# Kernel optimization log

Hardware: AMD Instinct MI355X
Metric: run time of the kernel (lower is better)

Reference implementation:

```python
import jax, jax.numpy as jnp
import numpy as np
from jax import lax

WINDOW_SIZE = 12
POOL = 4  # AvgPool2d(4): 12x12 -> 3x3

# 4 directional 3x3 kernels, stacked as [O=4, I=1, 3, 3]
_KERNELS = np.stack([
    np.array([[0, 0, 0], [-1, 1, 0], [0, 0, 0]], np.float32),  # left
    np.array([[0, 0, 0], [0, 1, -1], [0, 0, 0]], np.float32),  # right
    np.array([[0, -1, 0], [0, 1, 0], [0, 0, 0]], np.float32),  # up
    np.array([[0, 0, 0], [0, 1, 0], [0, -1, 0]], np.float32),  # down
])[:, None, :, :]


def setup_inputs() -> dict:
    key = jax.random.key(0)
    k1, k2 = jax.random.split(key)
    windows_num = 200000
    n = WINDOW_SIZE * WINDOW_SIZE * windows_num
    samples1 = jax.random.uniform(k1, (n, 3), dtype=jnp.float32)
    samples2 = jax.random.uniform(k2, (n, 3), dtype=jnp.float32)
    return {"samples1": samples1, "samples2": samples2, "windows_num": windows_num}


def _to_pooled(samples, windows_num):
    # [W*W*N, C] -> [W, W, N, C] -> [N, C, W, W]
    x = samples.reshape(WINDOW_SIZE, WINDOW_SIZE, windows_num, -1)
    x = jnp.transpose(x, (2, 3, 0, 1))
    # channel mean, keepdim -> [N, 1, W, W]
    m = jnp.mean(x, axis=1, keepdims=True)
    # AvgPool2d(4): [N,1,12,12] -> [N,1,3,3]
    hp = WINDOW_SIZE // POOL
    p = m.reshape(windows_num, 1, hp, POOL, hp, POOL).mean(axis=(3, 5))
    return p


def _dir_grads(x):
    # x: [N,1,3,3]; 4 directional 3x3 convs, padding=1 -> [N,4,3,3]
    k = jnp.asarray(_KERNELS)
    return lax.conv_general_dilated(
        x, k, window_strides=(1, 1), padding=[(1, 1), (1, 1)],
        dimension_numbers=("NCHW", "OIHW", "NCHW"))


def reference(samples1, samples2, windows_num):
    org_pool = _to_pooled(samples1, windows_num)
    enh_pool = _to_pooled(samples2, windows_num)
    d_org = _dir_grads(org_pool)
    d_enh = _dir_grads(enh_pool)
    # squared diff per direction, summed over the 4 directions -> [N,3,3]
    E = jnp.sum((d_org - d_enh) ** 2, axis=1)
    return jnp.mean(E)
```

## Files before the change

kernel.cpp:

```cpp
#include <hip/hip_runtime.h>

__global__ __launch_bounds__(256) void spa_kernel(
    const float* __restrict__ s1, const float* __restrict__ s2,
    float* __restrict__ out, int N, float scale) {
  const int lane = threadIdx.x & 63;
  const int rg   = threadIdx.x >> 6;
  const int win  = blockIdx.x * 64 + lane;

  float rowacc[3][3];
#pragma unroll
  for (int a = 0; a < 3; ++a)
#pragma unroll
    for (int b = 0; b < 3; ++b) rowacc[a][b] = 0.f;

  if (win < N) {
    const size_t stride = (size_t)N * 3u;
    const float* p1 = s1 + (size_t)win * 3u;
    const float* p2 = s2 + (size_t)win * 3u;
#pragma unroll
    for (int ii = 0; ii < 3; ++ii) {
      const int i = rg * 3 + ii;
      const float* q1 = p1 + (size_t)(i * 12) * stride;
      const float* q2 = p2 + (size_t)(i * 12) * stride;
#pragma unroll
      for (int j = 0; j < 12; ++j) {
        const float* a = q1 + (size_t)j * stride;
        const float* b = q2 + (size_t)j * stride;
        float d = (a[0] + a[1] + a[2]) - (b[0] + b[1] + b[2]);
        rowacc[ii][j >> 2] += d;
      }
    }
  }

  __shared__ float sRow[12][64][3];
#pragma unroll
  for (int ii = 0; ii < 3; ++ii) {
    const int i = rg * 3 + ii;
#pragma unroll
    for (int c = 0; c < 3; ++c) sRow[i][lane][c] = rowacc[ii][c];
  }
  __syncthreads();

  if (rg == 0) {
    float P[9];
#pragma unroll
    for (int p = 0; p < 3; ++p)
#pragma unroll
      for (int c = 0; c < 3; ++c) {
        float v = sRow[4 * p][lane][c] + sRow[4 * p + 1][lane][c] +
                  sRow[4 * p + 2][lane][c] + sRow[4 * p + 3][lane][c];
        P[p * 3 + c] = v * (1.0f / 48.0f);
      }

    float e = 0.f;
#pragma unroll
    for (int i = 0; i < 3; ++i) {
#pragma unroll
      for (int j = 0; j < 3; ++j) {
        float c = P[i * 3 + j];
        float l = (j > 0) ? P[i * 3 + j - 1] : 0.f;
        float r = (j < 2) ? P[i * 3 + j + 1] : 0.f;
        float u = (i > 0) ? P[(i - 1) * 3 + j] : 0.f;
        float d = (i < 2) ? P[(i + 1) * 3 + j] : 0.f;
        float dl = c - l, dr = c - r, du = c - u, dd = c - d;
        e += dl * dl + dr * dr + du * du + dd * dd;
      }
    }

#pragma unroll
    for (int off = 32; off > 0; off >>= 1) e += __shfl_down(e, off, 64);
    if (lane == 0) atomicAdd(out, e * scale);
  }
}

extern "C" void kernel_launch(void* const* d_in, const int* in_sizes, int n_in,
                              void* d_out, int out_size, void* d_ws, size_t ws_size,
                              hipStream_t stream) {
  const float* s1 = (const float*)d_in[0];
  const float* s2 = (const float*)d_in[1];
  float* out = (float*)d_out;
  int N = in_sizes[0] / (12 * 12 * 3);
  float scale = 1.0f / (9.0f * (float)N);
  hipMemsetAsync(d_out, 0, sizeof(float), stream);
  int blocks = (N + 63) / 64;
  spa_kernel<<<blocks, 256, 0, stream>>>(s1, s2, out, N, scale);
}
```

Baseline: 618.2 us.

## Split reduction into vectorized partial-sum kernel and finishing kernel via workspace

Replaces the single kernel with two passes. The first launches one thread per (pooled row-slab, group of 4 windows) and uses float4 loads to sum channel differences into a workspace. The second reads the 36 partial sums per window, computes the directional gradient energy and reduces. This aims for wider, better-coalesced memory access and more parallelism, at the cost of an extra workspace write and read plus a second launch; it falls back to the old kernel if the workspace is too small.

```diff
diff --git a/kernel.cpp b/kernel.cpp
--- a/kernel.cpp
+++ b/kernel.cpp
@@ -1,18 +1,111 @@
 #include <hip/hip_runtime.h>
 
-__global__ __launch_bounds__(256) void spa_kernel(
+
+__global__ __launch_bounds__(256) void spa_partial(
+    const float* __restrict__ s1, const float* __restrict__ s2,
+    float* __restrict__ ws, int N, int Q ) {
+  const long long t = (long long)blockIdx.x * blockDim.x + threadIdx.x;
+  const int s = (int)(t / Q);
+  const int q = (int)(t % Q);
+  if (s >= 36) return;
+  const int i = s / 3;
+  const int jc = s - i * 3;
+
+  float acc0 = 0.f, acc1 = 0.f, acc2 = 0.f, acc3 = 0.f;
+  const size_t slab = (size_t)N * 3u;
+
+  if (4 * q + 3 < N) {
+    const size_t off = (size_t)q * 12u;
+#pragma unroll
+    for (int jj = 0; jj < 4; ++jj) {
+      const int p = i * 12 + jc * 4 + jj;
+      const float4* a4 = (const float4*)(s1 + (size_t)p * slab + off);
+      const float4* b4 = (const float4*)(s2 + (size_t)p * slab + off);
+      float4 a0 = a4[0], a1 = a4[1], a2 = a4[2];
+      float4 b0 = b4[0], b1 = b4[1], b2 = b4[2];
+      float4 d0 = make_float4(a0.x - b0.x, a0.y - b0.y, a0.z - b0.z, a0.w - b0.w);
+      float4 d1 = make_float4(a1.x - b1.x, a1.y - b1.y, a1.z - b1.z, a1.w - b1.w);
+      float4 d2 = make_float4(a2.x - b2.x, a2.y - b2.y, a2.z - b2.z, a2.w - b2.w);
+      acc0 += d0.x + d0.y + d0.z;
+      acc1 += d0.w + d1.x + d1.y;
+      acc2 += d1.z + d1.w + d2.x;
+      acc3 += d2.y + d2.z + d2.w;
+    }
+    float4* w4 = (float4*)(ws + (size_t)s * N + (size_t)q * 4u);
+    *w4 = make_float4(acc0, acc1, acc2, acc3);
+  } else {
+    float acc[4] = {0.f, 0.f, 0.f, 0.f};
+#pragma unroll
+    for (int jj = 0; jj < 4; ++jj) {
+      const int p = i * 12 + jc * 4 + jj;
+      const float* a = s1 + (size_t)p * slab;
+      const float* b = s2 + (size_t)p * slab;
+      for (int w = 0; w < 4; ++w) {
+        const int n = 4 * q + w;
+        if (n < N) {
+          const size_t o = (size_t)n * 3u;
+          acc[w] += (a[o] + a[o + 1] + a[o + 2]) - (b[o] + b[o + 1] + b[o + 2]);
+        }
+      }
+    }
+    for (int w = 0; w < 4; ++w) {
+      const int n = 4 * q + w;
+      if (n < N) ws[(size_t)s * N + n] = acc[w];
+    }
+  }
+}
+
+__global__ __launch_bounds__(256) void spa_finish(
+    const float* __restrict__ ws, float* __restrict__ out, int N, float scale) {
+  const int n = blockIdx.x * blockDim.x + threadIdx.x;
+  float e = 0.f;
+  if (n < N) {
+    float P[9];
+#pragma unroll
+    for (int ip = 0; ip < 3; ++ip)
+#pragma unroll
+      for (int jc = 0; jc < 3; ++jc) {
+        float v = 0.f;
+#pragma unroll
+        for (int ii = 0; ii < 4; ++ii)
+          v += ws[(size_t)((4 * ip + ii) * 3 + jc) * N + n];
+        P[ip * 3 + jc] = v * (1.0f / 48.0f);
+      }
+#pragma unroll
+    for (int i = 0; i < 3; ++i) {
+#pragma unroll
+      for (int j = 0; j < 3; ++j) {
+        float c = P[i * 3 + j];
+        float l = (j > 0) ? P[i * 3 + j - 1] : 0.f;
+        float r = (j < 2) ? P[i * 3 + j + 1] : 0.f;
+        float u = (i > 0) ? P[(i - 1) * 3 + j] : 0.f;
+        float d = (i < 2) ? P[(i + 1) * 3 + j] : 0.f;
+        float dl = c - l, dr = c - r, du = c - u, dd = c - d;
+        e += dl * dl + dr * dr + du * du + dd * dd;
+      }
+    }
+  }
+#pragma unroll
+  for (int off = 32; off > 0; off >>= 1) e += __shfl_down(e, off, 64);
+  __shared__ float sm[4];
+  const int lane = threadIdx.x & 63;
+  const int wid = threadIdx.x >> 6;
+  if (lane == 0) sm[wid] = e;
+  __syncthreads();
+  if (threadIdx.x == 0) atomicAdd(out, (sm[0] + sm[1] + sm[2] + sm[3]) * scale);
+}
+
+__global__ __launch_bounds__(256) void spa_mono(
     const float* __restrict__ s1, const float* __restrict__ s2,
     float* __restrict__ out, int N, float scale) {
   const int lane = threadIdx.x & 63;
-  const int rg   = threadIdx.x >> 6;
-  const int win  = blockIdx.x * 64 + lane;
-
+  const int rg = threadIdx.x >> 6;
+  const int win = blockIdx.x * 64 + lane;
   float rowacc[3][3];
 #pragma unroll
   for (int a = 0; a < 3; ++a)
 #pragma unroll
     for (int b = 0; b < 3; ++b) rowacc[a][b] = 0.f;
-
   if (win < N) {
     const size_t stride = (size_t)N * 3u;
     const float* p1 = s1 + (size_t)win * 3u;
@@ -31,7 +124,6 @@
       }
     }
   }
-
   __shared__ float sRow[12][64][3];
 #pragma unroll
   for (int ii = 0; ii < 3; ++ii) {
@@ -40,7 +132,6 @@
     for (int c = 0; c < 3; ++c) sRow[i][lane][c] = rowacc[ii][c];
   }
   __syncthreads();
-
   if (rg == 0) {
     float P[9];
 #pragma unroll
@@ -51,7 +142,6 @@
                   sRow[4 * p + 2][lane][c] + sRow[4 * p + 3][lane][c];
         P[p * 3 + c] = v * (1.0f / 48.0f);
       }
-
     float e = 0.f;
 #pragma unroll
     for (int i = 0; i < 3; ++i) {
@@ -66,7 +156,6 @@
         e += dl * dl + dr * dr + du * du + dd * dd;
       }
     }
-
 #pragma unroll
     for (int off = 32; off > 0; off >>= 1) e += __shfl_down(e, off, 64);
     if (lane == 0) atomicAdd(out, e * scale);
@@ -79,9 +168,20 @@
   const float* s1 = (const float*)d_in[0];
   const float* s2 = (const float*)d_in[1];
   float* out = (float*)d_out;
-  int N = in_sizes[0] / (12 * 12 * 3);
-  float scale = 1.0f / (9.0f * (float)N);
+  const int N = in_sizes[0] / (12 * 12 * 3);
+  const float scale = 1.0f / (9.0f * (float)N);
   hipMemsetAsync(d_out, 0, sizeof(float), stream);
-  int blocks = (N + 63) / 64;
-  spa_kernel<<<blocks, 256, 0, stream>>>(s1, s2, out, N, scale);
+
+  const size_t ws_needed = (size_t)36 * (size_t)N * sizeof(float);
+  if (ws_size >= ws_needed) {
+    const int Q = (N + 3) / 4;
+    const long long threads = 36LL * Q;
+    const int blocksA = (int)((threads + 255) / 256);
+    spa_partial<<<blocksA, 256, 0, stream>>>(s1, s2, (float*)d_ws, N, Q);
+    const int blocksB = (N + 255) / 256;
+    spa_finish<<<blocksB, 256, 0, stream>>>((const float*)d_ws, out, N, scale);
+  } else {
+    const int blocks = (N + 63) / 64;
+    spa_mono<<<blocks, 256, 0, stream>>>(s1, s2, out, N, scale);
+  }
 }
```

Measured after the change: 681.3 us. +10.2%, slower.
